# Kernel optimization log

Measured on AMD Instinct MI355X. Metric: run time of the kernel, lower is better.

Reference implementation:

```python
import jax, jax.numpy as jnp
import numpy as np

B, L, D, E, H = 8, 2048, 1024, 8, 2048


def setup_inputs() -> dict:
    key = jax.random.key(0)
    ks = jax.random.split(key, 5)
    scale_in = 1.0 / np.sqrt(D)
    scale_h = 1.0 / np.sqrt(H)
    return {
        "x": jax.random.normal(ks[0], (B, L, D), dtype=jnp.float32),
        "Wg": jax.random.normal(ks[1], (D, E), dtype=jnp.float32) * scale_in,
        "bg": jnp.zeros((E,), dtype=jnp.float32),
        "W1": jax.random.normal(ks[2], (E, D, H), dtype=jnp.float32) * scale_in,
        "b1": jnp.zeros((E, H), dtype=jnp.float32),
        "W2": jax.random.normal(ks[3], (E, H, D), dtype=jnp.float32) * scale_h,
        "b2": jnp.zeros((E, D), dtype=jnp.float32),
    }


def reference(x, Wg, bg, W1, b1, W2, b2):
    # x: [B, L, D] -> tokens [N, D]
    Bs, Ls, Ds = x.shape
    x_flat = x.reshape(-1, Ds)                                   # [N, D]
    gate_logits = x_flat @ Wg + bg                               # [N, E]
    gate_weights = jax.nn.softmax(gate_logits, axis=-1)          # [N, E]
    # top-1 gate (torch.topk with k=1)
    top_idx = jnp.argmax(gate_weights, axis=-1)                  # [N]
    top_w = jnp.max(gate_weights, axis=-1)                       # [N]
    # dense all-expert compute (matches torch.stack over experts)
    hidden = jax.nn.relu(jnp.einsum('nd,edh->neh', x_flat, W1) + b1)  # [N, E, H]
    expert_outputs = jnp.einsum('neh,ehd->ned', hidden, W2) + b2     # [N, E, D]
    # gather the selected expert per token, scale by its gate weight
    selected = jnp.take_along_axis(expert_outputs, top_idx[:, None, None], axis=1)[:, 0, :]  # [N, D]
    out_flat = top_w[:, None] * selected                          # [N, D]
    out = out_flat.reshape(Bs, Ls, Ds)
    return out, gate_weights
```

## Files before the change

### kernel.cpp

```cpp
#include <hip/hip_runtime.h>
#include <hip/hip_bf16.h>

#define N_TOK 16384
#define D_DIM 1024
#define E_NUM 8
#define H_DIM 2048
#define MT 32
#define FFN_BLK 512

typedef __attribute__((ext_vector_type(8))) short short8;
typedef __attribute__((ext_vector_type(4))) float floatx4;

__device__ __forceinline__ unsigned short f2bf_bits(float f) {
    __hip_bfloat16 h = __float2bfloat16(f);
    return *reinterpret_cast<unsigned short*>(&h);
}

__device__ __forceinline__ void async16(const void* g, void* l) {
    __builtin_amdgcn_global_load_lds(
        (const __attribute__((address_space(1))) unsigned int*)g,
        (__attribute__((address_space(3))) unsigned int*)l,
        16, 0, 0);
}

__global__ __launch_bounds__(256) void moe_gate_kernel(
    const float* __restrict__ x,
    const float* __restrict__ Wg,
    const float* __restrict__ bg,
    float* __restrict__ gw_out,
    float* __restrict__ topw,
    int* __restrict__ topidx,
    unsigned short* __restrict__ xb) {
    int wave = (blockIdx.x * blockDim.x + threadIdx.x) >> 6;
    int lane = threadIdx.x & 63;
    if (wave >= N_TOK) return;
    const float* xr = x + (size_t)wave * D_DIM;

    float4 xv[4];
#pragma unroll
    for (int i = 0; i < 4; i++)
        xv[i] = *(const float4*)(xr + i * 256 + lane * 4);

#pragma unroll
    for (int i = 0; i < 4; i++) {
        ushort4 o;
        o.x = f2bf_bits(xv[i].x); o.y = f2bf_bits(xv[i].y);
        o.z = f2bf_bits(xv[i].z); o.w = f2bf_bits(xv[i].w);
        *(ushort4*)(xb + (size_t)wave * D_DIM + i * 256 + lane * 4) = o;
    }

    float acc[8];
#pragma unroll
    for (int e = 0; e < 8; e++) acc[e] = 0.f;

#pragma unroll
    for (int i = 0; i < 4; i++) {
        const float xs4[4] = {xv[i].x, xv[i].y, xv[i].z, xv[i].w};
        const float* wp = Wg + ((size_t)(i * 256) + lane * 4) * 8;
#pragma unroll
        for (int j = 0; j < 4; j++) {
            float4 w0 = *(const float4*)(wp + j * 8);
            float4 w1 = *(const float4*)(wp + j * 8 + 4);
            float s = xs4[j];
            acc[0] += s * w0.x; acc[1] += s * w0.y;
            acc[2] += s * w0.z; acc[3] += s * w0.w;
            acc[4] += s * w1.x; acc[5] += s * w1.y;
            acc[6] += s * w1.z; acc[7] += s * w1.w;
        }
    }
#pragma unroll
    for (int e = 0; e < 8; e++) {
#pragma unroll
        for (int off = 32; off > 0; off >>= 1)
            acc[e] += __shfl_xor(acc[e], off, 64);
    }
#pragma unroll
    for (int e = 0; e < 8; e++) acc[e] += bg[e];

    float mx = acc[0]; int am = 0;
#pragma unroll
    for (int e = 1; e < 8; e++) { if (acc[e] > mx) { mx = acc[e]; am = e; } }
    float w[8], s = 0.f;
#pragma unroll
    for (int e = 0; e < 8; e++) { w[e] = expf(acc[e] - mx); s += w[e]; }
    float inv = 1.f / s;
#pragma unroll
    for (int e = 0; e < 8; e++) w[e] *= inv;

    if (lane == 0) {
        float4 a = make_float4(w[0], w[1], w[2], w[3]);
        float4 b = make_float4(w[4], w[5], w[6], w[7]);
        *(float4*)(gw_out + (size_t)wave * 8)     = a;
        *(float4*)(gw_out + (size_t)wave * 8 + 4) = b;
        topw[wave]   = w[am];
        topidx[wave] = am;
    }
}

__global__ __launch_bounds__(256) void moe_hist_scan_kernel(
    const int* __restrict__ topidx,
    int* __restrict__ offsets,
    int* __restrict__ cursor) {
    __shared__ int part[256][8];
    int tid = threadIdx.x;
    int c0 = 0, c1 = 0, c2 = 0, c3 = 0, c4 = 0, c5 = 0, c6 = 0, c7 = 0;
    for (int i = 0; i < N_TOK / 256; i++) {
        int idx = topidx[tid + (i << 8)];
        c0 += (idx == 0); c1 += (idx == 1); c2 += (idx == 2); c3 += (idx == 3);
        c4 += (idx == 4); c5 += (idx == 5); c6 += (idx == 6); c7 += (idx == 7);
    }
    part[tid][0] = c0; part[tid][1] = c1; part[tid][2] = c2; part[tid][3] = c3;
    part[tid][4] = c4; part[tid][5] = c5; part[tid][6] = c6; part[tid][7] = c7;
    __syncthreads();
    for (int s = 128; s > 0; s >>= 1) {
        if (tid < s) {
#pragma unroll
            for (int e = 0; e < 8; e++) part[tid][e] += part[tid + s][e];
        }
        __syncthreads();
    }
    if (tid == 0) {
        int run = 0;
        for (int e = 0; e < 8; e++) {
            offsets[e] = run;
            cursor[e]  = run;
            run += part[0][e];
        }
        offsets[8] = run;
    }
}

__global__ __launch_bounds__(256) void moe_scatter_kernel(
    const int* __restrict__ topidx,
    int* __restrict__ cursor,
    int* __restrict__ toksort) {
    __shared__ int lcnt[8];
    __shared__ int lbase[8];
    int tid = threadIdx.x;
    int t = blockIdx.x * blockDim.x + tid;
    if (tid < 8) lcnt[tid] = 0;
    __syncthreads();
    int e = topidx[t];
    int r = atomicAdd(&lcnt[e], 1);
    __syncthreads();
    if (tid < 8) lbase[tid] = atomicAdd(&cursor[tid], lcnt[tid]);
    __syncthreads();
    toksort[lbase[e] + r] = t;
}

__global__ __launch_bounds__(256) void transpose_cast_kernel(
    const float* __restrict__ in, unsigned short* __restrict__ out,
    int R, int C) {
    __shared__ float tile[64][65];
    const float* inE = in + (size_t)blockIdx.z * R * C;
    unsigned short* outE = out + (size_t)blockIdx.z * R * C;
    int c0 = blockIdx.x << 6, r0 = blockIdx.y << 6;
    int tr = threadIdx.x >> 4;
    int tc = (threadIdx.x & 15) << 2;
#pragma unroll
    for (int i = 0; i < 4; i++) {
        int r = tr + (i << 4);
        float4 v = *(const float4*)(inE + (size_t)(r0 + r) * C + c0 + tc);
        tile[r][tc + 0] = v.x; tile[r][tc + 1] = v.y;
        tile[r][tc + 2] = v.z; tile[r][tc + 3] = v.w;
    }
    __syncthreads();
#pragma unroll
    for (int i = 0; i < 4; i++) {
        int c = tr + (i << 4);
        ushort4 o;
        o.x = f2bf_bits(tile[tc + 0][c]);
        o.y = f2bf_bits(tile[tc + 1][c]);
        o.z = f2bf_bits(tile[tc + 2][c]);
        o.w = f2bf_bits(tile[tc + 3][c]);
        *(ushort4*)(outE + (size_t)(c0 + c) * R + r0 + tc) = o;
    }
}

__global__ __launch_bounds__(256) void gather_sorted_kernel(
    const unsigned short* __restrict__ xb, const int* __restrict__ toksort,
    unsigned short* __restrict__ xs) {
    int p = (blockIdx.x << 1) + (threadIdx.x >> 7);
    int tok = toksort[p];
    int c = (threadIdx.x & 127) << 3;
    float4 v = *(const float4*)(xb + (size_t)tok * D_DIM + c);
    *(float4*)(xs + (size_t)p * D_DIM + c) = v;
}

__device__ __forceinline__ int find_tile(const int* offsets, int mt,
                                         int& row0, int& rows) {
    int cum = 0;
    for (int ee = 0; ee < E_NUM; ee++) {
        int o0 = offsets[ee], o1 = offsets[ee + 1];
        int tiles = (o1 - o0 + 127) >> 7;
        if (mt < cum + tiles) {
            row0 = o0 + ((mt - cum) << 7);
            rows = o1 - row0; if (rows > 128) rows = 128;
            return ee;
        }
        cum += tiles;
    }
    return -1;
}

__global__ __launch_bounds__(256) void moe_ffn1_mfma(
    const unsigned short* __restrict__ xs,
    const unsigned short* __restrict__ W1t,
    const float* __restrict__ b1,
    const int* __restrict__ offsets,
    unsigned short* __restrict__ hb) {

    __shared__ __align__(16) unsigned short As[128 * 32];
    __shared__ __align__(16) unsigned short Bs[128 * 32];

    int row0, rows;
    int e = find_tile(offsets, blockIdx.x, row0, rows);
    if (e < 0) return;
    int n0 = blockIdx.y << 7;

    int tid = threadIdx.x, l = tid & 63, w = tid >> 6;
    int wm = w & 1, wn = w >> 1;
    int lrow = l & 15, lq = l >> 4;
    const unsigned short* Be = W1t + (size_t)e * H_DIM * D_DIM;

    floatx4 acc[4][4];
#pragma unroll
    for (int mi = 0; mi < 4; mi++)
#pragma unroll
        for (int ni = 0; ni < 4; ni++) acc[mi][ni] = floatx4{0.f, 0.f, 0.f, 0.f};

    int srow = (w << 5) + (l >> 2);
    int koff = (l & 3) << 3;

    for (int kt = 0; kt < D_DIM / 32; kt++) {
        int kb = kt << 5;
        __syncthreads();
#pragma unroll
        for (int i = 0; i < 2; i++) {
            int r = srow + (i << 4);
            int p = row0 + r; if (p > N_TOK - 1) p = N_TOK - 1;
            async16(xs + (size_t)p * D_DIM + kb + koff,
                    As + (((w << 5) + (i << 4)) << 5));
            async16(Be + (size_t)(n0 + r) * D_DIM + kb + koff,
                    Bs + (((w << 5) + (i << 4)) << 5));
        }
        __syncthreads();
        short8 af[4], bfv[4];
#pragma unroll
        for (int mi = 0; mi < 4; mi++)
            af[mi] = *(const short8*)(As + (((wm << 6) + (mi << 4) + lrow) << 5) + (lq << 3));
#pragma unroll
        for (int ni = 0; ni < 4; ni++)
            bfv[ni] = *(const short8*)(Bs + (((wn << 6) + (ni << 4) + lrow) << 5) + (lq << 3));
#pragma unroll
        for (int mi = 0; mi < 4; mi++)
#pragma unroll
            for (int ni = 0; ni < 4; ni++)
                acc[mi][ni] = __builtin_amdgcn_mfma_f32_16x16x32_bf16(
                    af[mi], bfv[ni], acc[mi][ni], 0, 0, 0);
    }

#pragma unroll
    for (int ni = 0; ni < 4; ni++) {
        int h = n0 + (wn << 6) + (ni << 4) + lrow;
        float bias = b1[e * H_DIM + h];
#pragma unroll
        for (int mi = 0; mi < 4; mi++) {
#pragma unroll
            for (int r = 0; r < 4; r++) {
                int row = (wm << 6) + (mi << 4) + (lq << 2) + r;
                if (row < rows) {
                    float v = acc[mi][ni][r] + bias;
                    v = v > 0.f ? v : 0.f;
                    hb[(size_t)(row0 + row) * H_DIM + h] = f2bf_bits(v);
                }
            }
        }
    }
}

__global__ __launch_bounds__(256) void moe_ffn2_mfma(
    const unsigned short* __restrict__ hb,
    const unsigned short* __restrict__ W2t,
    const float* __restrict__ b2,
    const int* __restrict__ offsets,
    const int* __restrict__ toksort,
    const float* __restrict__ topw,
    float* __restrict__ out) {

    __shared__ __align__(16) unsigned short As[128 * 32];
    __shared__ __align__(16) unsigned short Bs[128 * 32];

    int row0, rows;
    int e = find_tile(offsets, blockIdx.x, row0, rows);
    if (e < 0) return;
    int n0 = blockIdx.y << 7;

    int tid = threadIdx.x, l = tid & 63, w = tid >> 6;
    int wm = w & 1, wn = w >> 1;
    int lrow = l & 15, lq = l >> 4;
    const unsigned short* Be = W2t + (size_t)e * D_DIM * H_DIM;

    floatx4 acc[4][4];
#pragma unroll
    for (int mi = 0; mi < 4; mi++)
#pragma unroll
        for (int ni = 0; ni < 4; ni++) acc[mi][ni] = floatx4{0.f, 0.f, 0.f, 0.f};

    int srow = (w << 5) + (l >> 2);
    int koff = (l & 3) << 3;

    for (int kt = 0; kt < H_DIM / 32; kt++) {
        int kb = kt << 5;
        __syncthreads();
#pragma unroll
        for (int i = 0; i < 2; i++) {
            int r = srow + (i << 4);
            int p = row0 + r; if (p > N_TOK - 1) p = N_TOK - 1;
            async16(hb + (size_t)p * H_DIM + kb + koff,
                    As + (((w << 5) + (i << 4)) << 5));
            async16(Be + (size_t)(n0 + r) * H_DIM + kb + koff,
                    Bs + (((w << 5) + (i << 4)) << 5));
        }
        __syncthreads();
        short8 af[4], bfv[4];
#pragma unroll
        for (int mi = 0; mi < 4; mi++)
            af[mi] = *(const short8*)(As + (((wm << 6) + (mi << 4) + lrow) << 5) + (lq << 3));
#pragma unroll
        for (int ni = 0; ni < 4; ni++)
            bfv[ni] = *(const short8*)(Bs + (((wn << 6) + (ni << 4) + lrow) << 5) + (lq << 3));
#pragma unroll
        for (int mi = 0; mi < 4; mi++)
#pragma unroll
            for (int ni = 0; ni < 4; ni++)
                acc[mi][ni] = __builtin_amdgcn_mfma_f32_16x16x32_bf16(
                    af[mi], bfv[ni], acc[mi][ni], 0, 0, 0);
    }

    float bias[4];
#pragma unroll
    for (int ni = 0; ni < 4; ni++)
        bias[ni] = b2[e * D_DIM + n0 + (wn << 6) + (ni << 4) + lrow];

#pragma unroll
    for (int mi = 0; mi < 4; mi++) {
#pragma unroll
        for (int r = 0; r < 4; r++) {
            int row = (wm << 6) + (mi << 4) + (lq << 2) + r;
            if (row < rows) {
                int p = row0 + row;
                int tok = toksort[p];
                float tw = topw[tok];
#pragma unroll
                for (int ni = 0; ni < 4; ni++) {
                    int d = n0 + (wn << 6) + (ni << 4) + lrow;
                    out[(size_t)tok * D_DIM + d] = tw * (acc[mi][ni][r] + bias[ni]);
                }
            }
        }
    }
}

__global__ __launch_bounds__(FFN_BLK, 2) void moe_ffn_kernel(
    const float* __restrict__ x,
    const float* __restrict__ W1, const float* __restrict__ b1,
    const float* __restrict__ W2, const float* __restrict__ b2,
    const int* __restrict__ offsets,
    const int* __restrict__ toksort,
    const float* __restrict__ topw,
    float* __restrict__ out) {

    __shared__ __align__(16) unsigned short h1c[MT * 1024];
    float* xs = (float*)h1c;

    int bid = blockIdx.x;
    int e = -1, row0 = 0, rows = 0, cum = 0;
    for (int ee = 0; ee < E_NUM; ee++) {
        int o0 = offsets[ee], o1 = offsets[ee + 1];
        int tiles = (o1 - o0 + MT - 1) / MT;
        if (bid < cum + tiles) {
            e = ee;
            row0 = o0 + (bid - cum) * MT;
            rows = (o1 - row0 < MT) ? (o1 - row0) : MT;
            break;
        }
        cum += tiles;
    }
    if (e < 0) return;

    int tid = threadIdx.x;
    const float* W1e = W1 + (size_t)e * D_DIM * H_DIM;
    const float* W2e = W2 + (size_t)e * H_DIM * D_DIM;

    int m_st = tid >> 4;
    int j_st = tid & 15;
    int m_cl = (m_st < rows) ? m_st : (rows - 1);
    int tok_st = toksort[row0 + m_cl];

    float acc2x[MT], acc2y[MT];
#pragma unroll
    for (int m = 0; m < MT; m++) { acc2x[m] = 0.f; acc2y[m] = 0.f; }

    int d0 = tid * 2;

    for (int half = 0; half < 2; half++) {
        int ha = half * 1024 + tid;
        int hb_ = ha + 512;

        float a1a[MT], a1b[MT];
#pragma unroll
        for (int m = 0; m < MT; m++) { a1a[m] = 0.f; a1b[m] = 0.f; }

        for (int dc = 0; dc < 8; dc++) {
            __syncthreads();
            {
                const float4* src =
                    (const float4*)(x + (size_t)tok_st * D_DIM + dc * 128 + j_st * 8);
                float4 v0 = src[0], v1 = src[1];
                float4* dst = (float4*)(xs + m_st * 128 + j_st * 8);
                dst[0] = v0; dst[1] = v1;
            }
            __syncthreads();
            const float* w1pa = W1e + (size_t)(dc * 128) * H_DIM + ha;
            const float* w1pb = W1e + (size_t)(dc * 128) * H_DIM + hb_;
            for (int d2 = 0; d2 < 64; d2++) {
                float wa0 = w1pa[0], wa1 = w1pa[H_DIM];
                float wb0 = w1pb[0], wb1 = w1pb[H_DIM];
                w1pa += 2 * H_DIM; w1pb += 2 * H_DIM;
#pragma unroll
                for (int m = 0; m < MT; m++) {
                    float2 xv = *(const float2*)(xs + m * 128 + d2 * 2);
                    a1a[m] += xv.x * wa0; a1a[m] += xv.y * wa1;
                    a1b[m] += xv.x * wb0; a1b[m] += xv.y * wb1;
                }
            }
        }

        float bba = b1[e * H_DIM + ha];
        float bbb = b1[e * H_DIM + hb_];
        __syncthreads();
#pragma unroll
        for (int m = 0; m < MT; m++) {
            float va = a1a[m] + bba; va = va > 0.f ? va : 0.f;
            float vb = a1b[m] + bbb; vb = vb > 0.f ? vb : 0.f;
            h1c[m * 1024 + tid]       = f2bf_bits(va);
            h1c[m * 1024 + 512 + tid] = f2bf_bits(vb);
        }
        __syncthreads();

        const float* w2p = W2e + (size_t)(half * 1024) * D_DIM + d0;
        for (int hh = 0; hh < 1024; hh += 2) {
            float2 w2a = *(const float2*)(w2p);
            float2 w2b = *(const float2*)(w2p + D_DIM);
            w2p += 2 * D_DIM;
#pragma unroll
            for (int m = 0; m < MT; m++) {
                unsigned int u = *(const unsigned int*)(h1c + m * 1024 + hh);
                float h0  = __uint_as_float(u << 16);
                float h1v = __uint_as_float(u & 0xffff0000u);
                acc2x[m] += h0 * w2a.x; acc2x[m] += h1v * w2b.x;
                acc2y[m] += h0 * w2a.y; acc2y[m] += h1v * w2b.y;
            }
        }
    }

    float bb0 = b2[e * D_DIM + d0];
    float bb1 = b2[e * D_DIM + d0 + 1];
#pragma unroll
    for (int m = 0; m < MT; m++) {
        if (m < rows) {
            int tok  = toksort[row0 + m];
            float tw = topw[tok];
            float2 o;
            o.x = tw * (acc2x[m] + bb0);
            o.y = tw * (acc2y[m] + bb1);
            *(float2*)(out + (size_t)tok * D_DIM + d0) = o;
        }
    }
}

extern "C" void kernel_launch(void* const* d_in, const int* in_sizes, int n_in,
                              void* d_out, int out_size, void* d_ws, size_t ws_size,
                              hipStream_t stream) {
    const float* x  = (const float*)d_in[0];
    const float* Wg = (const float*)d_in[1];
    const float* bg = (const float*)d_in[2];
    const float* W1 = (const float*)d_in[3];
    const float* b1 = (const float*)d_in[4];
    const float* W2 = (const float*)d_in[5];
    const float* b2 = (const float*)d_in[6];

    float* out = (float*)d_out;
    float* gw  = out + (size_t)N_TOK * D_DIM;

    char* ws = (char*)d_ws;
    int*   counts  = (int*)ws;
    int*   cursor  = counts + 8;
    int*   offsets = cursor + 8;
    int*   topidx  = (int*)(ws + 128);
    float* topw    = (float*)(ws + 128 + 4 * (size_t)N_TOK);
    int*   toksort = (int*)(ws + 128 + 8 * (size_t)N_TOK);

    const size_t off_xs  = 256ull << 10;
    const size_t off_w1t = off_xs  + (32ull << 20);
    const size_t off_w2t = off_w1t + (32ull << 20);
    const size_t off_hb  = off_w2t + (32ull << 20);
    const size_t off_xb  = off_hb;
    const size_t need    = off_hb  + (64ull << 20);

    if (ws_size >= need) {
        unsigned short* xs  = (unsigned short*)(ws + off_xs);
        unsigned short* W1t = (unsigned short*)(ws + off_w1t);
        unsigned short* W2t = (unsigned short*)(ws + off_w2t);
        unsigned short* hb  = (unsigned short*)(ws + off_hb);
        unsigned short* xb  = (unsigned short*)(ws + off_xb);

        moe_gate_kernel<<<N_TOK / 4, 256, 0, stream>>>(
            x, Wg, bg, gw, topw, topidx, xb);
        moe_hist_scan_kernel<<<1, 256, 0, stream>>>(topidx, offsets, cursor);
        moe_scatter_kernel<<<N_TOK / 256, 256, 0, stream>>>(topidx, cursor, toksort);

        transpose_cast_kernel<<<dim3(H_DIM / 64, D_DIM / 64, E_NUM), 256, 0, stream>>>(
            W1, W1t, D_DIM, H_DIM);
        transpose_cast_kernel<<<dim3(D_DIM / 64, H_DIM / 64, E_NUM), 256, 0, stream>>>(
            W2, W2t, H_DIM, D_DIM);
        gather_sorted_kernel<<<N_TOK / 2, 256, 0, stream>>>(xb, toksort, xs);

        moe_ffn1_mfma<<<dim3(N_TOK / 128 + E_NUM, H_DIM / 128), 256, 0, stream>>>(
            xs, W1t, b1, offsets, hb);
        moe_ffn2_mfma<<<dim3(N_TOK / 128 + E_NUM, D_DIM / 128), 256, 0, stream>>>(
            hb, W2t, b2, offsets, toksort, topw, out);
    } else {
        unsigned short* xb = (unsigned short*)(ws + (256ull << 10));
        moe_gate_kernel<<<N_TOK / 4, 256, 0, stream>>>(
            x, Wg, bg, gw, topw, topidx, xb);
        moe_hist_scan_kernel<<<1, 256, 0, stream>>>(topidx, offsets, cursor);
        moe_scatter_kernel<<<N_TOK / 256, 256, 0, stream>>>(topidx, cursor, toksort);
        moe_ffn_kernel<<<N_TOK / MT + E_NUM, FFN_BLK, 0, stream>>>(
            x, W1, b1, W2, b2, offsets, toksort, topw, out);
    }
}
```

Baseline: 537.1 us.

## Fuse gate with weight transposes, fuse scatter with gather, swizzle GEMM blocks

The gate kernel and both weight transpose-casts now run as a single launch, and the separate xb bf16 buffer is dropped. The scatter step now also casts x to bf16 and writes it straight into sorted order, which removes the gather kernel and one pass over the activations. The two FFN GEMMs gain an XCD-aware block swizzle, and FFN1 stages its output tile through LDS so it can write coalesced 16-byte stores. The transpose writes are widened to 8-element vectors and the histogram reads int4. The cost is more LDS in FFN1 and a gather loop that runs serially over 64 tokens per block.

```diff
diff --git a/kernel.cpp b/kernel.cpp
--- a/kernel.cpp
+++ b/kernel.cpp
@@ -23,15 +23,61 @@
         16, 0, 0);
 }
 
-__global__ __launch_bounds__(256) void moe_gate_kernel(
+__global__ __launch_bounds__(256) void moe_gate_transpose_fused(
     const float* __restrict__ x,
     const float* __restrict__ Wg,
     const float* __restrict__ bg,
     float* __restrict__ gw_out,
     float* __restrict__ topw,
     int* __restrict__ topidx,
-    unsigned short* __restrict__ xb) {
-    int wave = (blockIdx.x * blockDim.x + threadIdx.x) >> 6;
+    const float* __restrict__ W1,
+    const float* __restrict__ W2,
+    unsigned short* __restrict__ W1t,
+    unsigned short* __restrict__ W2t) {
+
+    __shared__ float tile[64][65];
+
+    if (blockIdx.x < 8192) {
+        int id = blockIdx.x;
+        const float* in; unsigned short* out; int R, C, cx, ry, e;
+        if (id < 4096) {
+            e = id >> 9; int t = id & 511;
+            in = W1; out = W1t; R = 1024; C = 2048;
+            cx = t & 31; ry = t >> 5;
+        } else {
+            id -= 4096;
+            e = id >> 9; int t = id & 511;
+            in = W2; out = W2t; R = 2048; C = 1024;
+            cx = t & 15; ry = t >> 4;
+        }
+        const float* inE = in + (size_t)e * 2097152;
+        unsigned short* outE = out + (size_t)e * 2097152;
+        int c0 = cx << 6, r0 = ry << 6;
+        int tr = threadIdx.x >> 4;
+        int tc = (threadIdx.x & 15) << 2;
+#pragma unroll
+        for (int i = 0; i < 4; i++) {
+            int r = tr + (i << 4);
+            float4 v = *(const float4*)(inE + (size_t)(r0 + r) * C + c0 + tc);
+            tile[r][tc + 0] = v.x; tile[r][tc + 1] = v.y;
+            tile[r][tc + 2] = v.z; tile[r][tc + 3] = v.w;
+        }
+        __syncthreads();
+#pragma unroll
+        for (int it = 0; it < 2; it++) {
+            int task = threadIdx.x + (it << 8);
+            int c = task >> 3, rr = (task & 7) << 3;
+            short8 o;
+#pragma unroll
+            for (int j = 0; j < 8; j++)
+                ((unsigned short*)&o)[j] = f2bf_bits(tile[rr + j][c]);
+            *(short8*)(outE + (size_t)(c0 + c) * R + r0 + rr) = o;
+        }
+        return;
+    }
+
+    int bid = blockIdx.x - 8192;
+    int wave = ((bid << 8) + threadIdx.x) >> 6;
     int lane = threadIdx.x & 63;
     if (wave >= N_TOK) return;
     const float* xr = x + (size_t)wave * D_DIM;
@@ -40,14 +86,6 @@
 #pragma unroll
     for (int i = 0; i < 4; i++)
         xv[i] = *(const float4*)(xr + i * 256 + lane * 4);
-
-#pragma unroll
-    for (int i = 0; i < 4; i++) {
-        ushort4 o;
-        o.x = f2bf_bits(xv[i].x); o.y = f2bf_bits(xv[i].y);
-        o.z = f2bf_bits(xv[i].z); o.w = f2bf_bits(xv[i].w);
-        *(ushort4*)(xb + (size_t)wave * D_DIM + i * 256 + lane * 4) = o;
-    }
 
     float acc[8];
 #pragma unroll
@@ -97,6 +135,70 @@
     }
 }
 
+__global__ __launch_bounds__(256) void moe_gate_kernel(
+    const float* __restrict__ x,
+    const float* __restrict__ Wg,
+    const float* __restrict__ bg,
+    float* __restrict__ gw_out,
+    float* __restrict__ topw,
+    int* __restrict__ topidx) {
+    int wave = (blockIdx.x * blockDim.x + threadIdx.x) >> 6;
+    int lane = threadIdx.x & 63;
+    if (wave >= N_TOK) return;
+    const float* xr = x + (size_t)wave * D_DIM;
+
+    float4 xv[4];
+#pragma unroll
+    for (int i = 0; i < 4; i++)
+        xv[i] = *(const float4*)(xr + i * 256 + lane * 4);
+
+    float acc[8];
+#pragma unroll
+    for (int e = 0; e < 8; e++) acc[e] = 0.f;
+#pragma unroll
+    for (int i = 0; i < 4; i++) {
+        const float xs4[4] = {xv[i].x, xv[i].y, xv[i].z, xv[i].w};
+        const float* wp = Wg + ((size_t)(i * 256) + lane * 4) * 8;
+#pragma unroll
+        for (int j = 0; j < 4; j++) {
+            float4 w0 = *(const float4*)(wp + j * 8);
+            float4 w1 = *(const float4*)(wp + j * 8 + 4);
+            float s = xs4[j];
+            acc[0] += s * w0.x; acc[1] += s * w0.y;
+            acc[2] += s * w0.z; acc[3] += s * w0.w;
+            acc[4] += s * w1.x; acc[5] += s * w1.y;
+            acc[6] += s * w1.z; acc[7] += s * w1.w;
+        }
+    }
+#pragma unroll
+    for (int e = 0; e < 8; e++) {
+#pragma unroll
+        for (int off = 32; off > 0; off >>= 1)
+            acc[e] += __shfl_xor(acc[e], off, 64);
+    }
+#pragma unroll
+    for (int e = 0; e < 8; e++) acc[e] += bg[e];
+
+    float mx = acc[0]; int am = 0;
+#pragma unroll
+    for (int e = 1; e < 8; e++) { if (acc[e] > mx) { mx = acc[e]; am = e; } }
+    float w[8], s = 0.f;
+#pragma unroll
+    for (int e = 0; e < 8; e++) { w[e] = expf(acc[e] - mx); s += w[e]; }
+    float inv = 1.f / s;
+#pragma unroll
+    for (int e = 0; e < 8; e++) w[e] *= inv;
+
+    if (lane == 0) {
+        float4 a = make_float4(w[0], w[1], w[2], w[3]);
+        float4 b = make_float4(w[4], w[5], w[6], w[7]);
+        *(float4*)(gw_out + (size_t)wave * 8)     = a;
+        *(float4*)(gw_out + (size_t)wave * 8 + 4) = b;
+        topw[wave]   = w[am];
+        topidx[wave] = am;
+    }
+}
+
 __global__ __launch_bounds__(256) void moe_hist_scan_kernel(
     const int* __restrict__ topidx,
     int* __restrict__ offsets,
@@ -104,10 +206,15 @@
     __shared__ int part[256][8];
     int tid = threadIdx.x;
     int c0 = 0, c1 = 0, c2 = 0, c3 = 0, c4 = 0, c5 = 0, c6 = 0, c7 = 0;
-    for (int i = 0; i < N_TOK / 256; i++) {
-        int idx = topidx[tid + (i << 8)];
-        c0 += (idx == 0); c1 += (idx == 1); c2 += (idx == 2); c3 += (idx == 3);
-        c4 += (idx == 4); c5 += (idx == 5); c6 += (idx == 6); c7 += (idx == 7);
+    const int4* tp = (const int4*)topidx;
+    for (int i = 0; i < N_TOK / 1024; i++) {
+        int4 v = tp[tid + (i << 8)];
+#pragma unroll
+        for (int j = 0; j < 4; j++) {
+            int idx = (&v.x)[j];
+            c0 += (idx == 0); c1 += (idx == 1); c2 += (idx == 2); c3 += (idx == 3);
+            c4 += (idx == 4); c5 += (idx == 5); c6 += (idx == 6); c7 += (idx == 7);
+        }
     }
     part[tid][0] = c0; part[tid][1] = c1; part[tid][2] = c2; part[tid][3] = c3;
     part[tid][4] = c4; part[tid][5] = c5; part[tid][6] = c6; part[tid][7] = c7;
@@ -127,6 +234,44 @@
             run += part[0][e];
         }
         offsets[8] = run;
+    }
+}
+
+__global__ __launch_bounds__(256) void moe_scatter_gather(
+    const float* __restrict__ x,
+    const int* __restrict__ topidx,
+    int* __restrict__ cursor,
+    int* __restrict__ toksort,
+    unsigned short* __restrict__ xs) {
+    __shared__ int lcnt[8];
+    __shared__ int lbase[8];
+    __shared__ int s_pos[64];
+    int tid = threadIdx.x;
+    int base = blockIdx.x << 6;
+    if (tid < 8) lcnt[tid] = 0;
+    __syncthreads();
+    int e = 0, r = 0;
+    if (tid < 64) {
+        e = topidx[base + tid];
+        r = atomicAdd(&lcnt[e], 1);
+    }
+    __syncthreads();
+    if (tid < 8) lbase[tid] = atomicAdd(&cursor[tid], lcnt[tid]);
+    __syncthreads();
+    if (tid < 64) {
+        int p = lbase[e] + r;
+        toksort[p] = base + tid;
+        s_pos[tid] = p;
+    }
+    __syncthreads();
+    for (int rr = 0; rr < 64; rr++) {
+        int tok = base + rr;
+        int p = s_pos[rr];
+        float4 v = *(const float4*)(x + (size_t)tok * D_DIM + (tid << 2));
+        ushort4 o;
+        o.x = f2bf_bits(v.x); o.y = f2bf_bits(v.y);
+        o.z = f2bf_bits(v.z); o.w = f2bf_bits(v.w);
+        *(ushort4*)(xs + (size_t)p * D_DIM + (tid << 2)) = o;
     }
 }
 
@@ -146,45 +291,6 @@
     if (tid < 8) lbase[tid] = atomicAdd(&cursor[tid], lcnt[tid]);
     __syncthreads();
     toksort[lbase[e] + r] = t;
-}
-
-__global__ __launch_bounds__(256) void transpose_cast_kernel(
-    const float* __restrict__ in, unsigned short* __restrict__ out,
-    int R, int C) {
-    __shared__ float tile[64][65];
-    const float* inE = in + (size_t)blockIdx.z * R * C;
-    unsigned short* outE = out + (size_t)blockIdx.z * R * C;
-    int c0 = blockIdx.x << 6, r0 = blockIdx.y << 6;
-    int tr = threadIdx.x >> 4;
-    int tc = (threadIdx.x & 15) << 2;
-#pragma unroll
-    for (int i = 0; i < 4; i++) {
-        int r = tr + (i << 4);
-        float4 v = *(const float4*)(inE + (size_t)(r0 + r) * C + c0 + tc);
-        tile[r][tc + 0] = v.x; tile[r][tc + 1] = v.y;
-        tile[r][tc + 2] = v.z; tile[r][tc + 3] = v.w;
-    }
-    __syncthreads();
-#pragma unroll
-    for (int i = 0; i < 4; i++) {
-        int c = tr + (i << 4);
-        ushort4 o;
-        o.x = f2bf_bits(tile[tc + 0][c]);
-        o.y = f2bf_bits(tile[tc + 1][c]);
-        o.z = f2bf_bits(tile[tc + 2][c]);
-        o.w = f2bf_bits(tile[tc + 3][c]);
-        *(ushort4*)(outE + (size_t)(c0 + c) * R + r0 + tc) = o;
-    }
-}
-
-__global__ __launch_bounds__(256) void gather_sorted_kernel(
-    const unsigned short* __restrict__ xb, const int* __restrict__ toksort,
-    unsigned short* __restrict__ xs) {
-    int p = (blockIdx.x << 1) + (threadIdx.x >> 7);
-    int tok = toksort[p];
-    int c = (threadIdx.x & 127) << 3;
-    float4 v = *(const float4*)(xb + (size_t)tok * D_DIM + c);
-    *(float4*)(xs + (size_t)p * D_DIM + c) = v;
 }
 
 __device__ __forceinline__ int find_tile(const int* offsets, int mt,
@@ -203,6 +309,15 @@
     return -1;
 }
 
+__device__ __forceinline__ void xcd_swizzle(int& bx, int& by) {
+    int nwgx = gridDim.x;
+    int id = blockIdx.y * nwgx + blockIdx.x;
+    int nwg = nwgx * gridDim.y;
+    int cpx = nwg >> 3;
+    int swz = (id & 7) * cpx + (id >> 3);
+    bx = swz % nwgx; by = swz / nwgx;
+}
+
 __global__ __launch_bounds__(256) void moe_ffn1_mfma(
     const unsigned short* __restrict__ xs,
     const unsigned short* __restrict__ W1t,
@@ -210,13 +325,17 @@
     const int* __restrict__ offsets,
     unsigned short* __restrict__ hb) {
 
-    __shared__ __align__(16) unsigned short As[128 * 32];
-    __shared__ __align__(16) unsigned short Bs[128 * 32];
+    __shared__ __align__(16) unsigned short LDS[128 * 132];
+    unsigned short* As = LDS;
+    unsigned short* Bs = LDS + 4096;
+
+    int bx, by;
+    xcd_swizzle(bx, by);
 
     int row0, rows;
-    int e = find_tile(offsets, blockIdx.x, row0, rows);
+    int e = find_tile(offsets, bx, row0, rows);
     if (e < 0) return;
-    int n0 = blockIdx.y << 7;
+    int n0 = by << 7;
 
     int tid = threadIdx.x, l = tid & 63, w = tid >> 6;
     int wm = w & 1, wn = w >> 1;
@@ -260,22 +379,30 @@
                     af[mi], bfv[ni], acc[mi][ni], 0, 0, 0);
     }
 
+    __syncthreads();
 #pragma unroll
     for (int ni = 0; ni < 4; ni++) {
-        int h = n0 + (wn << 6) + (ni << 4) + lrow;
-        float bias = b1[e * H_DIM + h];
+        int cl = (wn << 6) + (ni << 4) + lrow;
+        float bias = b1[e * H_DIM + n0 + cl];
 #pragma unroll
         for (int mi = 0; mi < 4; mi++) {
 #pragma unroll
             for (int r = 0; r < 4; r++) {
-                int row = (wm << 6) + (mi << 4) + (lq << 2) + r;
-                if (row < rows) {
-                    float v = acc[mi][ni][r] + bias;
-                    v = v > 0.f ? v : 0.f;
-                    hb[(size_t)(row0 + row) * H_DIM + h] = f2bf_bits(v);
-                }
+                int rl = (wm << 6) + (mi << 4) + (lq << 2) + r;
+                float v = acc[mi][ni][r] + bias;
+                v = v > 0.f ? v : 0.f;
+                LDS[rl * 132 + cl] = f2bf_bits(v);
             }
         }
+    }
+    __syncthreads();
+    int trow = tid >> 1, tcol = (tid & 1) << 6;
+    if (trow < rows) {
+        unsigned short* dst = hb + (size_t)(row0 + trow) * H_DIM + n0 + tcol;
+        const unsigned short* src = LDS + trow * 132 + tcol;
+#pragma unroll
+        for (int i2 = 0; i2 < 8; i2++)
+            *(short8*)(dst + i2 * 8) = *(const short8*)(src + i2 * 8);
     }
 }
 
@@ -291,10 +418,13 @@
     __shared__ __align__(16) unsigned short As[128 * 32];
     __shared__ __align__(16) unsigned short Bs[128 * 32];
 
+    int bx, by;
+    xcd_swizzle(bx, by);
+
     int row0, rows;
-    int e = find_tile(offsets, blockIdx.x, row0, rows);
+    int e = find_tile(offsets, bx, row0, rows);
     if (e < 0) return;
-    int n0 = blockIdx.y << 7;
+    int n0 = by << 7;
 
     int tid = threadIdx.x, l = tid & 63, w = tid >> 6;
     int wm = w & 1, wn = w >> 1;
@@ -506,7 +636,6 @@
     const size_t off_w1t = off_xs  + (32ull << 20);
     const size_t off_w2t = off_w1t + (32ull << 20);
     const size_t off_hb  = off_w2t + (32ull << 20);
-    const size_t off_xb  = off_hb;
     const size_t need    = off_hb  + (64ull << 20);
 
     if (ws_size >= need) {
@@ -514,27 +643,20 @@
         unsigned short* W1t = (unsigned short*)(ws + off_w1t);
         unsigned short* W2t = (unsigned short*)(ws + off_w2t);
         unsigned short* hb  = (unsigned short*)(ws + off_hb);
-        unsigned short* xb  = (unsigned short*)(ws + off_xb);
-
-        moe_gate_kernel<<<N_TOK / 4, 256, 0, stream>>>(
-            x, Wg, bg, gw, topw, topidx, xb);
+
+        moe_gate_transpose_fused<<<12288, 256, 0, stream>>>(
+            x, Wg, bg, gw, topw, topidx, W1, W2, W1t, W2t);
         moe_hist_scan_kernel<<<1, 256, 0, stream>>>(topidx, offsets, cursor);
-        moe_scatter_kernel<<<N_TOK / 256, 256, 0, stream>>>(topidx, cursor, toksort);
-
-        transpose_cast_kernel<<<dim3(H_DIM / 64, D_DIM / 64, E_NUM), 256, 0, stream>>>(
-            W1, W1t, D_DIM, H_DIM);
-        transpose_cast_kernel<<<dim3(D_DIM / 64, H_DIM / 64, E_NUM), 256, 0, stream>>>(
-            W2, W2t, H_DIM, D_DIM);
-        gather_sorted_kernel<<<N_TOK / 2, 256, 0, stream>>>(xb, toksort, xs);
+        moe_scatter_gather<<<N_TOK / 64, 256, 0, stream>>>(
+            x, topidx, cursor, toksort, xs);
 
         moe_ffn1_mfma<<<dim3(N_TOK / 128 + E_NUM, H_DIM / 128), 256, 0, stream>>>(
             xs, W1t, b1, offsets, hb);
         moe_ffn2_mfma<<<dim3(N_TOK / 128 + E_NUM, D_DIM / 128), 256, 0, stream>>>(
             hb, W2t, b2, offsets, toksort, topw, out);
     } else {
-        unsigned short* xb = (unsigned short*)(ws + (256ull << 10));
         moe_gate_kernel<<<N_TOK / 4, 256, 0, stream>>>(
-            x, Wg, bg, gw, topw, topidx, xb);
+            x, Wg, bg, gw, topw, topidx);
         moe_hist_scan_kernel<<<1, 256, 0, stream>>>(topidx, offsets, cursor);
         moe_scatter_kernel<<<N_TOK / 256, 256, 0, stream>>>(topidx, cursor, toksort);
         moe_ffn_kernel<<<N_TOK / MT + E_NUM, FFN_BLK, 0, stream>>>(
```

New measurement: 533.2 us. No clear change (-0.7%).
